# Optimization experiments

Hardware: AMD Instinct MI355X
Metric: run time of the kernel (lower is better)

## Reference

```python
import jax, jax.numpy as jnp
import numpy as np

B, T, C = 2, 2048, 1024
N_HEAD = 16
HEAD_DIM = C // N_HEAD


def setup_inputs() -> dict:
    key = jax.random.key(0)
    k1, k2, k3 = jax.random.split(key, 3)
    s = 1.0 / np.sqrt(C)
    return {
        "x": jax.random.normal(k1, (B, T, C), dtype=jnp.float32),
        "w_qkv": jax.random.normal(k2, (C, 3 * C), dtype=jnp.float32) * s,
        "b_qkv": jnp.zeros((3 * C,), dtype=jnp.float32),
        "w_out": jax.random.normal(k3, (C, C), dtype=jnp.float32) * s,
        "b_out": jnp.zeros((C,), dtype=jnp.float32),
    }


def reference(x, w_qkv, b_qkv, w_out, b_out):
    b, t, c = x.shape
    qkv = x @ w_qkv + b_qkv                                   # [B,T,3C]
    # Faithful to torch: view(B,T,H,3*hd).transpose(1,2) then split last dim
    qkv = qkv.reshape(b, t, N_HEAD, 3 * HEAD_DIM).transpose(0, 2, 1, 3)  # [B,H,T,3hd]
    q, k, v = jnp.split(qkv, 3, axis=-1)                      # each [B,H,T,hd]
    att = jnp.einsum("bhqd,bhkd->bhqk", q, k) / np.sqrt(HEAD_DIM)
    causal = jnp.tril(jnp.ones((t, t), dtype=bool))
    att = jnp.where(causal[None, None], att, -jnp.inf)
    att = jax.nn.softmax(att, axis=-1)                        # dropout p=0 (eval)
    y = jnp.einsum("bhqk,bhkd->bhqd", att, v)                 # [B,H,T,hd]
    y = y.transpose(0, 2, 1, 3).reshape(b, t, c)
    return y @ w_out + b_out
```

## Files before the change

kernel.cpp:

```cpp
#include <hip/hip_runtime.h>


#define T_SEQ 2048
#define C_DIM 1024
#define NH    16
#define HD    64
#define BT    4096

typedef short bf16x8 __attribute__((ext_vector_type(8)));
typedef float floatx4 __attribute__((ext_vector_type(4)));

static __device__ __forceinline__ unsigned short f2bf(float f) {
    union { float f; unsigned u; } v; v.f = f;
    unsigned u = v.u;
    return (unsigned short)((u + 0x7FFFu + ((u >> 16) & 1u)) >> 16);
}
static __device__ __forceinline__ float bf2f(unsigned short u) {
    union { unsigned u; float f; } v; v.u = ((unsigned)u) << 16; return v.f;
}

static __device__ __forceinline__ void gl2lds16(const void* g, void* l) {
    __builtin_amdgcn_global_load_lds(
        (const __attribute__((address_space(1))) unsigned int*)g,
        (__attribute__((address_space(3))) unsigned int*)l, 16, 0, 0);
}

static __device__ __forceinline__ void transpose_body(float (*tile)[65],
                                                      const float* __restrict__ W,
                                                      unsigned short* __restrict__ Wt,
                                                      int K, int N, int bx, int by) {
    const int k0 = by << 6;
    const int n0 = bx << 6;
    const int rr = threadIdx.x >> 4;
    const int cc = (threadIdx.x & 15) << 2;
#pragma unroll
    for (int i = 0; i < 4; i++) {
        int r = rr + (i << 4);
        *(float4*)&tile[r][cc] = *(const float4*)(W + (size_t)(k0 + r) * N + n0 + cc);
    }
    __syncthreads();
#pragma unroll
    for (int i = 0; i < 4; i++) {
        int nr = rr + (i << 4);
        ushort4 o;
        o.x = f2bf(tile[cc + 0][nr]);
        o.y = f2bf(tile[cc + 1][nr]);
        o.z = f2bf(tile[cc + 2][nr]);
        o.w = f2bf(tile[cc + 3][nr]);
        *(ushort4*)(Wt + (size_t)(n0 + nr) * K + k0 + cc) = o;
    }
}

__global__ __launch_bounds__(256) void prep(const float* __restrict__ x,
                                            unsigned short* __restrict__ xb,
                                            const float* __restrict__ w_qkv,
                                            unsigned short* __restrict__ wqkvT,
                                            const float* __restrict__ w_out,
                                            unsigned short* __restrict__ woutT) {
    __shared__ float tile[64][65];
    const int bx = blockIdx.x;
    if (bx < 1024) {
        int i = (bx * 256 + threadIdx.x) * 4;
        const int n = BT * C_DIM;
        const int stride = 1024 * 1024;
        for (; i < n; i += stride) {
            float4 f = *(const float4*)(x + i);
            ushort4 o;
            o.x = f2bf(f.x); o.y = f2bf(f.y); o.z = f2bf(f.z); o.w = f2bf(f.w);
            *(ushort4*)(xb + i) = o;
        }
    } else if (bx < 1024 + 768) {
        int b = bx - 1024;
        transpose_body(tile, w_qkv, wqkvT, 1024, 3072, b % 48, b / 48);
    } else {
        int b = bx - 1024 - 768;
        transpose_body(tile, w_out, woutT, 1024, 1024, b % 16, b / 16);
    }
}

__global__ __launch_bounds__(256) void transp_v(const unsigned short* __restrict__ vb,
                                                unsigned short* __restrict__ vt) {
    __shared__ unsigned short tile[64][68];
    const int t0 = blockIdx.x << 6;
    const int bh = blockIdx.y;
    const size_t base = (size_t)bh * T_SEQ * HD;
    const int r = threadIdx.x >> 3;
    const int c = (threadIdx.x & 7) << 3;
#pragma unroll
    for (int i = 0; i < 2; i++) {
        const unsigned short* src = vb + base + (size_t)(t0 + r + (i << 5)) * HD + c;
        ushort4 u0 = *(const ushort4*)src;
        ushort4 u1 = *(const ushort4*)(src + 4);
        *(ushort4*)&tile[r + (i << 5)][c] = u0;
        *(ushort4*)&tile[r + (i << 5)][c + 4] = u1;
    }
    __syncthreads();
#pragma unroll
    for (int i = 0; i < 2; i++) {
        int s = threadIdx.x + (i << 8);
        int d = s >> 3;
        int tc = (s & 7) << 3;
        ushort4 o0, o1;
        o0.x = tile[tc + 0][d]; o0.y = tile[tc + 1][d];
        o0.z = tile[tc + 2][d]; o0.w = tile[tc + 3][d];
        o1.x = tile[tc + 4][d]; o1.y = tile[tc + 5][d];
        o1.z = tile[tc + 6][d]; o1.w = tile[tc + 7][d];
        unsigned short* dst = vt + ((size_t)bh * HD + d) * T_SEQ + t0 + tc;
        *(ushort4*)dst = o0;
        *(ushort4*)(dst + 4) = o1;
    }
}

#define GEMM_CORE(A_, Bt_, K_)                                                      \
    __shared__ short As[128 * 64];                                                  \
    __shared__ short Bs[128 * 64];                                                  \
    const int tid  = threadIdx.x;                                                   \
    const int lane = tid & 63, wave = tid >> 6;                                     \
    const int ln   = lane & 15, quad = lane >> 4;                                   \
    const int wm   = wave & 1,  wn   = wave >> 1;                                   \
    const int row0 = blockIdx.y << 7;                                               \
    const int col0 = blockIdx.x << 7;                                               \
    floatx4 acc[4][4];                                                              \
    _Pragma("unroll")                                                               \
    for (int i = 0; i < 4; i++)                                                     \
        _Pragma("unroll")                                                           \
        for (int j = 0; j < 4; j++) acc[i][j] = (floatx4){0.f, 0.f, 0.f, 0.f};      \
    for (int k0 = 0; k0 < K_; k0 += 64) {                                           \
        _Pragma("unroll")                                                           \
        for (int i = 0; i < 4; i++) {                                               \
            int c = (i << 8) + tid;                                                 \
            int r = c >> 3;                                                         \
            int gsrc = (c & 7) ^ (r & 7);                                           \
            gl2lds16(A_  + (size_t)(row0 + r) * K_ + k0 + (gsrc << 3), &As[c << 3]); \
            gl2lds16(Bt_ + (size_t)(col0 + r) * K_ + k0 + (gsrc << 3), &Bs[c << 3]); \
        }                                                                           \
        __syncthreads();                                                            \
        _Pragma("unroll")                                                           \
        for (int half = 0; half < 2; half++) {                                      \
            bf16x8 af[4], bfr[4];                                                   \
            _Pragma("unroll")                                                       \
            for (int t4 = 0; t4 < 4; t4++) {                                        \
                int ra = (wm << 6) + (t4 << 4) + ln;                                \
                int rb = (wn << 6) + (t4 << 4) + ln;                                \
                int g  = (half << 2) + quad;                                        \
                af[t4]  = *(bf16x8*)&As[((ra << 3) + (g ^ (ra & 7))) << 3];         \
                bfr[t4] = *(bf16x8*)&Bs[((rb << 3) + (g ^ (rb & 7))) << 3];         \
            }                                                                       \
            _Pragma("unroll")                                                       \
            for (int mt = 0; mt < 4; mt++)                                          \
                _Pragma("unroll")                                                   \
                for (int nt = 0; nt < 4; nt++)                                      \
                    acc[mt][nt] = __builtin_amdgcn_mfma_f32_16x16x32_bf16(af[mt], bfr[nt], acc[mt][nt], 0, 0, 0); \
        }                                                                           \
        __syncthreads();                                                            \
    }

__global__ __launch_bounds__(256) void gemm_qkv(const unsigned short* __restrict__ A,
                                                const unsigned short* __restrict__ Bt,
                                                const float* __restrict__ bias,
                                                unsigned short* __restrict__ qb,
                                                unsigned short* __restrict__ kb,
                                                unsigned short* __restrict__ vb) {
    GEMM_CORE(A, Bt, 1024)
#pragma unroll
    for (int mt = 0; mt < 4; mt++) {
#pragma unroll
        for (int nt = 0; nt < 4; nt++) {
            int n = col0 + (wn << 6) + (nt << 4) + ln;
            int h = n / 192, r = n % 192;
            int sel = r >> 6, d = r & 63;
            float bv = bias[n];
#pragma unroll
            for (int e = 0; e < 4; e++) {
                int m = row0 + (wm << 6) + (mt << 4) + (quad << 2) + e;
                int b = m >> 11, t = m & 2047;
                float val = acc[mt][nt][e] + bv;
                size_t idx = (((size_t)(b * NH + h)) * T_SEQ + t) * HD + d;
                if (sel == 0)
                    qb[idx] = f2bf(val * 0.125f);
                else if (sel == 1)
                    kb[idx] = f2bf(val);
                else
                    vb[idx] = f2bf(val);
            }
        }
    }
}

__global__ __launch_bounds__(256) void gemm_out(const unsigned short* __restrict__ A,
                                                const unsigned short* __restrict__ Bt,
                                                const float* __restrict__ bias,
                                                float* __restrict__ out) {
    const int K = 1024, N = 1024;
    __shared__ short As[128 * 64];
    __shared__ short Bs[64 * 64];
    const int tid  = threadIdx.x;
    const int lane = tid & 63, wave = tid >> 6;
    const int ln   = lane & 15, quad = lane >> 4;
    const int wm   = wave & 1,  wn   = wave >> 1;
    const int row0 = blockIdx.y << 7;
    const int col0 = blockIdx.x << 6;
    floatx4 acc[4][2];
#pragma unroll
    for (int i = 0; i < 4; i++)
#pragma unroll
        for (int j = 0; j < 2; j++) acc[i][j] = (floatx4){0.f, 0.f, 0.f, 0.f};
    for (int k0 = 0; k0 < K; k0 += 64) {
#pragma unroll
        for (int i = 0; i < 4; i++) {
            int c = (i << 8) + tid;
            int r = c >> 3;
            int gsrc = (c & 7) ^ (r & 7);
            gl2lds16(A + (size_t)(row0 + r) * K + k0 + (gsrc << 3), &As[c << 3]);
        }
#pragma unroll
        for (int i = 0; i < 2; i++) {
            int c = (i << 8) + tid;
            int r = c >> 3;
            int gsrc = (c & 7) ^ (r & 7);
            gl2lds16(Bt + (size_t)(col0 + r) * K + k0 + (gsrc << 3), &Bs[c << 3]);
        }
        __syncthreads();
#pragma unroll
        for (int half = 0; half < 2; half++) {
            bf16x8 af[4], bfr[2];
#pragma unroll
            for (int t4 = 0; t4 < 4; t4++) {
                int ra = (wm << 6) + (t4 << 4) + ln;
                int g  = (half << 2) + quad;
                af[t4] = *(bf16x8*)&As[((ra << 3) + (g ^ (ra & 7))) << 3];
            }
#pragma unroll
            for (int t2 = 0; t2 < 2; t2++) {
                int rb = (wn << 5) + (t2 << 4) + ln;
                int g  = (half << 2) + quad;
                bfr[t2] = *(bf16x8*)&Bs[((rb << 3) + (g ^ (rb & 7))) << 3];
            }
#pragma unroll
            for (int mt = 0; mt < 4; mt++)
#pragma unroll
                for (int nt = 0; nt < 2; nt++)
                    acc[mt][nt] = __builtin_amdgcn_mfma_f32_16x16x32_bf16(af[mt], bfr[nt], acc[mt][nt], 0, 0, 0);
        }
        __syncthreads();
    }
#pragma unroll
    for (int mt = 0; mt < 4; mt++) {
#pragma unroll
        for (int nt = 0; nt < 2; nt++) {
            int n = col0 + (wn << 5) + (nt << 4) + ln;
            float bv = bias[n];
#pragma unroll
            for (int e = 0; e < 4; e++) {
                int m = row0 + (wm << 6) + (mt << 4) + (quad << 2) + e;
                out[(size_t)m * N + n] = acc[mt][nt][e] + bv;
            }
        }
    }
}

__global__ __launch_bounds__(256) void attn_p1(const unsigned short* __restrict__ qb,
                                               const unsigned short* __restrict__ kb,
                                               const unsigned short* __restrict__ vt,
                                               unsigned short* __restrict__ y,
                                               unsigned short* __restrict__ po,
                                               float* __restrict__ pm,
                                               float* __restrict__ pl) {
    __shared__ short Ks[64][68];
    __shared__ short Vs[64][68];
    __shared__ short QP[64][68];
    const int tid  = threadIdx.x;
    const int w    = tid >> 6, lane = tid & 63;
    const int ln   = lane & 15, quad = lane >> 4;
    const int bx   = blockIdx.x;
    int qt, c;
    if (bx < 32)      { qt = 31 - bx;        c = 0; }
    else if (bx < 56) { qt = 31 - (bx - 32); c = 1; }
    else if (bx < 72) { qt = 31 - (bx - 56); c = 2; }
    else              { qt = 31 - (bx - 72); c = 3; }
    const int kt_lo = c << 3;
    const int kt_hi = (kt_lo + 7 < qt) ? (kt_lo + 7) : qt;
    const int nc    = (qt >> 3) + 1;
    const bool fin  = (nc == 1);
    const int bh   = blockIdx.y;
    const size_t base = (size_t)bh * T_SEQ * HD;
    const int q0   = qt << 6;
    const int sb   = q0 + (w << 4);
    const float NEG_INF = -__builtin_inff();

    const int sr = tid >> 3;
    const int sc = (tid & 7) << 3;

    const unsigned short* qrow = qb + base + (size_t)(q0 + (w << 4) + ln) * HD;
    bf16x8 bq0 = *(const bf16x8*)(qrow + (quad << 3));
    bf16x8 bq1 = *(const bf16x8*)(qrow + 32 + (quad << 3));

    bf16x8 kreg[2], vreg[2];
    const int kk0 = kt_lo << 6;
#pragma unroll
    for (int i = 0; i < 2; i++) {
        kreg[i] = *(const bf16x8*)(kb + base + (size_t)(kk0 + sr + (i << 5)) * HD + sc);
        vreg[i] = *(const bf16x8*)(vt + base + (size_t)(sr + (i << 5)) * T_SEQ + kk0 + sc);
    }

    floatx4 o[4];
#pragma unroll
    for (int nt = 0; nt < 4; nt++) o[nt] = (floatx4){0.f, 0.f, 0.f, 0.f};
    float m_prev = NEG_INF, l_run = 0.f;

    for (int kt = kt_lo; kt <= kt_hi; kt++) {
        const int k0 = kt << 6;
        __syncthreads();
#pragma unroll
        for (int i = 0; i < 2; i++) {
            *(bf16x8*)&Ks[sr + (i << 5)][sc] = kreg[i];
            *(bf16x8*)&Vs[sr + (i << 5)][sc] = vreg[i];
        }
        __syncthreads();
        if (kt < kt_hi) {
            const int kn = k0 + 64;
#pragma unroll
            for (int i = 0; i < 2; i++) {
                kreg[i] = *(const bf16x8*)(kb + base + (size_t)(kn + sr + (i << 5)) * HD + sc);
                vreg[i] = *(const bf16x8*)(vt + base + (size_t)(sr + (i << 5)) * T_SEQ + kn + sc);
            }
        }

        const bool diag  = (kt == qt);
        const int  nlive = diag ? w : 3;

        floatx4 st[4];
#pragma unroll
        for (int ktl = 0; ktl < 4; ktl++) {
            if (ktl <= nlive) {
                bf16x8 a0 = *(bf16x8*)&Ks[(ktl << 4) + ln][quad << 3];
                bf16x8 a1 = *(bf16x8*)&Ks[(ktl << 4) + ln][32 + (quad << 3)];
                floatx4 acc = (floatx4){0.f, 0.f, 0.f, 0.f};
                acc = __builtin_amdgcn_mfma_f32_16x16x32_bf16(a0, bq0, acc, 0, 0, 0);
                acc = __builtin_amdgcn_mfma_f32_16x16x32_bf16(a1, bq1, acc, 0, 0, 0);
                st[ktl] = acc;
            }
        }
        if (diag) {
#pragma unroll
            for (int ktl = 0; ktl < 4; ktl++) {
                if (ktl <= nlive) {
#pragma unroll
                    for (int e = 0; e < 4; e++) {
                        int kg = k0 + (ktl << 4) + (quad << 2) + e;
                        if (kg > sb + ln) st[ktl][e] = NEG_INF;
                    }
                }
            }
        }

        float mx = NEG_INF;
#pragma unroll
        for (int ktl = 0; ktl < 4; ktl++)
            if (ktl <= nlive) {
#pragma unroll
                for (int e = 0; e < 4; e++) mx = fmaxf(mx, st[ktl][e]);
            }
        mx = fmaxf(mx, __shfl_xor(mx, 16));
        mx = fmaxf(mx, __shfl_xor(mx, 32));
        float m_new = fmaxf(m_prev, mx);
        float alpha = __expf(m_prev - m_new);
        float psum = 0.f;
#pragma unroll
        for (int ktl = 0; ktl < 4; ktl++)
            if (ktl <= nlive) {
#pragma unroll
                for (int e = 0; e < 4; e++) {
                    float p = __expf(st[ktl][e] - m_new);
                    st[ktl][e] = p;
                    psum += p;
                }
            }
        psum += __shfl_xor(psum, 16);
        psum += __shfl_xor(psum, 32);
        l_run = l_run * alpha + psum;
        m_prev = m_new;

#pragma unroll
        for (int ktl = 0; ktl < 4; ktl++) {
            ushort4 pw;
            if (ktl <= nlive) {
                pw.x = f2bf(st[ktl][0]); pw.y = f2bf(st[ktl][1]);
                pw.z = f2bf(st[ktl][2]); pw.w = f2bf(st[ktl][3]);
            } else {
                pw.x = 0; pw.y = 0; pw.z = 0; pw.w = 0;
            }
            *(ushort4*)&QP[(w << 4) + ln][(ktl << 4) + (quad << 2)] = pw;
        }

        float arow[4];
#pragma unroll
        for (int e = 0; e < 4; e++) arow[e] = __shfl(alpha, (quad << 2) + e);
#pragma unroll
        for (int nt = 0; nt < 4; nt++)
#pragma unroll
            for (int e = 0; e < 4; e++) o[nt][e] *= arow[e];

        bf16x8 ap0 = *(bf16x8*)&QP[(w << 4) + ln][quad << 3];
        bf16x8 ap1 = *(bf16x8*)&QP[(w << 4) + ln][32 + (quad << 3)];
#pragma unroll
        for (int nt = 0; nt < 4; nt++) {
            bf16x8 v0 = *(bf16x8*)&Vs[(nt << 4) + ln][quad << 3];
            bf16x8 v1 = *(bf16x8*)&Vs[(nt << 4) + ln][32 + (quad << 3)];
            o[nt] = __builtin_amdgcn_mfma_f32_16x16x32_bf16(ap0, v0, o[nt], 0, 0, 0);
            o[nt] = __builtin_amdgcn_mfma_f32_16x16x32_bf16(ap1, v1, o[nt], 0, 0, 0);
        }
    }

    if (fin) {
        float linv[4];
#pragma unroll
        for (int e = 0; e < 4; e++) linv[e] = 1.0f / __shfl(l_run, (quad << 2) + e);
        const int b = bh >> 4, h = bh & 15;
#pragma unroll
        for (int e = 0; e < 4; e++) {
            int t = sb + (quad << 2) + e;
            unsigned short* yrow = y + ((size_t)b * T_SEQ + t) * C_DIM + h * HD;
#pragma unroll
            for (int nt = 0; nt < 4; nt++)
                yrow[(nt << 4) + ln] = f2bf(o[nt][e] * linv[e]);
        }
    } else {
        int cb;
        if (qt < 16)      cb = (qt - 8) * 2;
        else if (qt < 24) cb = 16 + (qt - 16) * 3;
        else              cb = 40 + (qt - 24) * 4;
        const int slot = bh * 72 + cb + c;
        if (quad == 0) {
            pm[(slot << 6) + (w << 4) + ln] = m_prev;
            pl[(slot << 6) + (w << 4) + ln] = l_run;
        }
#pragma unroll
        for (int e = 0; e < 4; e++) {
            int q = (w << 4) + (quad << 2) + e;
            unsigned short* porow = po + (((size_t)slot << 6) + q) * HD;
#pragma unroll
            for (int nt = 0; nt < 4; nt++)
                porow[(nt << 4) + ln] = f2bf(o[nt][e]);
        }
    }
}

__global__ __launch_bounds__(256) void attn_p2(const unsigned short* __restrict__ po,
                                               const float* __restrict__ pm,
                                               const float* __restrict__ pl,
                                               unsigned short* __restrict__ y) {
    const int qt = 8 + blockIdx.x;
    const int bh = blockIdx.y;
    const int nc = (qt >> 3) + 1;
    int cb;
    if (qt < 16)      cb = (qt - 8) * 2;
    else if (qt < 24) cb = 16 + (qt - 16) * 3;
    else              cb = 40 + (qt - 24) * 4;
    const int slot0 = bh * 72 + cb;
    const int tid = threadIdx.x;
    const int q  = tid >> 2;
    const int d0 = (tid & 3) << 4;
    const float NEG_INF = -__builtin_inff();

    float mv[4], lv[4];
#pragma unroll
    for (int cc = 0; cc < 4; cc++) {
        if (cc < nc) {
            mv[cc] = pm[((slot0 + cc) << 6) + q];
            lv[cc] = pl[((slot0 + cc) << 6) + q];
        } else {
            mv[cc] = NEG_INF; lv[cc] = 0.f;
        }
    }
    float m = fmaxf(fmaxf(mv[0], mv[1]), fmaxf(mv[2], mv[3]));
    float a[4];
    float L = 0.f;
#pragma unroll
    for (int cc = 0; cc < 4; cc++) {
        a[cc] = __expf(mv[cc] - m);
        L += lv[cc] * a[cc];
    }
    const float inv = 1.0f / L;
#pragma unroll
    for (int cc = 0; cc < 4; cc++) a[cc] *= inv;

    float acc[16];
#pragma unroll
    for (int i = 0; i < 16; i++) acc[i] = 0.f;
#pragma unroll
    for (int cc = 0; cc < 4; cc++) {
        if (cc < nc) {
            const unsigned short* r = po + (((size_t)(slot0 + cc)) << 12) + (q << 6) + d0;
            const float ac = a[cc];
#pragma unroll
            for (int i = 0; i < 4; i++) {
                ushort4 u = *(const ushort4*)(r + (i << 2));
                acc[(i << 2) + 0] += ac * bf2f(u.x);
                acc[(i << 2) + 1] += ac * bf2f(u.y);
                acc[(i << 2) + 2] += ac * bf2f(u.z);
                acc[(i << 2) + 3] += ac * bf2f(u.w);
            }
        }
    }

    const int b = bh >> 4, h = bh & 15;
    const int t = (qt << 6) + q;
    unsigned short* yrow = y + ((size_t)b * T_SEQ + t) * C_DIM + h * HD + d0;
#pragma unroll
    for (int i = 0; i < 4; i++) {
        ushort4 ow;
        ow.x = f2bf(acc[(i << 2) + 0]);
        ow.y = f2bf(acc[(i << 2) + 1]);
        ow.z = f2bf(acc[(i << 2) + 2]);
        ow.w = f2bf(acc[(i << 2) + 3]);
        *(ushort4*)(yrow + (i << 2)) = ow;
    }
}

extern "C" void kernel_launch(void* const* d_in, const int* in_sizes, int n_in,
                              void* d_out, int out_size, void* d_ws, size_t ws_size,
                              hipStream_t stream) {
    (void)in_sizes; (void)n_in; (void)out_size; (void)ws_size;
    const float* x     = (const float*)d_in[0];
    const float* w_qkv = (const float*)d_in[1];
    const float* b_qkv = (const float*)d_in[2];
    const float* w_out = (const float*)d_in[3];
    const float* b_out = (const float*)d_in[4];
    float* out = (float*)d_out;

    char* ws = (char*)d_ws;
    unsigned short* qb    = (unsigned short*)ws;
    unsigned short* kb    = (unsigned short*)(ws + ((size_t)8  << 20));
    unsigned short* vt    = (unsigned short*)(ws + ((size_t)16 << 20));
    unsigned short* xb    = (unsigned short*)(ws + ((size_t)24 << 20));
    unsigned short* yb    = xb;
    unsigned short* woutT = (unsigned short*)(ws + ((size_t)32 << 20));
    unsigned short* vb    = (unsigned short*)(ws + ((size_t)34 << 20));
    unsigned short* wqkvT = (unsigned short*)(ws + ((size_t)42 << 20));
    unsigned short* po    = (unsigned short*)(ws + ((size_t)34 << 20));
    float*          pm    = (float*)(ws + ((size_t)52 << 20));
    float*          pl    = (float*)(ws + ((size_t)52 << 20) + (640 << 10));

    prep    <<<2048, 256, 0, stream>>>(x, xb, w_qkv, wqkvT, w_out, woutT);
    gemm_qkv<<<dim3(24, 32), 256, 0, stream>>>(xb, wqkvT, b_qkv, qb, kb, vb);
    transp_v<<<dim3(32, 32), 256, 0, stream>>>(vb, vt);
    attn_p1 <<<dim3(80, 32), 256, 0, stream>>>(qb, kb, vt, yb, po, pm, pl);
    attn_p2 <<<dim3(24, 32), 256, 0, stream>>>(po, pm, pl, yb);
    gemm_out<<<dim3(16, 32), 256, 0, stream>>>(yb, woutT, b_out, out);
}
```

Before: 206.7 us.

## Process two query tiles per attention block to reuse K/V tiles

Each attention block now handles 128 query rows (two 64-row sub-tiles) against every loaded K/V tile, which halves global K/V loads and LDS staging per query. The grid shrinks from 80x32 to 40x32 blocks, and the split-KV partial layout and combine kernel are re-indexed for 128-row slots. In exchange, register pressure goes up from the doubled accumulators and there are fewer blocks to spread across the GPU's compute units.

```diff
diff --git a/kernel.cpp b/kernel.cpp
--- a/kernel.cpp
+++ b/kernel.cpp
@@ -268,32 +268,36 @@
                                                float* __restrict__ pl) {
     __shared__ short Ks[64][68];
     __shared__ short Vs[64][68];
-    __shared__ short QP[64][68];
+    __shared__ short QP[2][64][68];
     const int tid  = threadIdx.x;
     const int w    = tid >> 6, lane = tid & 63;
     const int ln   = lane & 15, quad = lane >> 4;
     const int bx   = blockIdx.x;
-    int qt, c;
-    if (bx < 32)      { qt = 31 - bx;        c = 0; }
-    else if (bx < 56) { qt = 31 - (bx - 32); c = 1; }
-    else if (bx < 72) { qt = 31 - (bx - 56); c = 2; }
-    else              { qt = 31 - (bx - 72); c = 3; }
+    int qt2, c;
+    if (bx < 16)      { qt2 = 15 - bx;        c = 0; }
+    else if (bx < 28) { qt2 = 15 - (bx - 16); c = 1; }
+    else if (bx < 36) { qt2 = 15 - (bx - 28); c = 2; }
+    else              { qt2 = 15 - (bx - 36); c = 3; }
     const int kt_lo = c << 3;
-    const int kt_hi = (kt_lo + 7 < qt) ? (kt_lo + 7) : qt;
-    const int nc    = (qt >> 3) + 1;
+    const int qtB   = (qt2 << 1) + 1;
+    const int kt_hi = (kt_lo + 7 < qtB) ? (kt_lo + 7) : qtB;
+    const int nc    = ((qt2 << 1) + 9) >> 3;
     const bool fin  = (nc == 1);
     const int bh   = blockIdx.y;
     const size_t base = (size_t)bh * T_SEQ * HD;
-    const int q0   = qt << 6;
-    const int sb   = q0 + (w << 4);
+    const int q0   = qt2 << 7;
     const float NEG_INF = -__builtin_inff();
 
     const int sr = tid >> 3;
     const int sc = (tid & 7) << 3;
 
-    const unsigned short* qrow = qb + base + (size_t)(q0 + (w << 4) + ln) * HD;
-    bf16x8 bq0 = *(const bf16x8*)(qrow + (quad << 3));
-    bf16x8 bq1 = *(const bf16x8*)(qrow + 32 + (quad << 3));
+    bf16x8 bq[2][2];
+#pragma unroll
+    for (int s = 0; s < 2; s++) {
+        const unsigned short* qrow = qb + base + (size_t)(q0 + (s << 6) + (w << 4) + ln) * HD;
+        bq[s][0] = *(const bf16x8*)(qrow + (quad << 3));
+        bq[s][1] = *(const bf16x8*)(qrow + 32 + (quad << 3));
+    }
 
     bf16x8 kreg[2], vreg[2];
     const int kk0 = kt_lo << 6;
@@ -303,10 +307,13 @@
         vreg[i] = *(const bf16x8*)(vt + base + (size_t)(sr + (i << 5)) * T_SEQ + kk0 + sc);
     }
 
-    floatx4 o[4];
-#pragma unroll
-    for (int nt = 0; nt < 4; nt++) o[nt] = (floatx4){0.f, 0.f, 0.f, 0.f};
-    float m_prev = NEG_INF, l_run = 0.f;
+    floatx4 o[2][4];
+#pragma unroll
+    for (int s = 0; s < 2; s++)
+#pragma unroll
+        for (int nt = 0; nt < 4; nt++) o[s][nt] = (floatx4){0.f, 0.f, 0.f, 0.f};
+    float m_prev[2] = {NEG_INF, NEG_INF};
+    float l_run[2]  = {0.f, 0.f};
 
     for (int kt = kt_lo; kt <= kt_hi; kt++) {
         const int k0 = kt << 6;
@@ -326,122 +333,134 @@
             }
         }
 
-        const bool diag  = (kt == qt);
-        const int  nlive = diag ? w : 3;
-
-        floatx4 st[4];
-#pragma unroll
-        for (int ktl = 0; ktl < 4; ktl++) {
-            if (ktl <= nlive) {
-                bf16x8 a0 = *(bf16x8*)&Ks[(ktl << 4) + ln][quad << 3];
-                bf16x8 a1 = *(bf16x8*)&Ks[(ktl << 4) + ln][32 + (quad << 3)];
-                floatx4 acc = (floatx4){0.f, 0.f, 0.f, 0.f};
-                acc = __builtin_amdgcn_mfma_f32_16x16x32_bf16(a0, bq0, acc, 0, 0, 0);
-                acc = __builtin_amdgcn_mfma_f32_16x16x32_bf16(a1, bq1, acc, 0, 0, 0);
-                st[ktl] = acc;
-            }
-        }
-        if (diag) {
+#pragma unroll
+        for (int s = 0; s < 2; s++) {
+            const int qts = (qt2 << 1) + s;
+            if (kt > qts) continue;
+            const bool diag  = (kt == qts);
+            const int  nlive = diag ? w : 3;
+            const int  sb    = q0 + (s << 6) + (w << 4);
+
+            floatx4 st[4];
 #pragma unroll
             for (int ktl = 0; ktl < 4; ktl++) {
                 if (ktl <= nlive) {
-#pragma unroll
-                    for (int e = 0; e < 4; e++) {
-                        int kg = k0 + (ktl << 4) + (quad << 2) + e;
-                        if (kg > sb + ln) st[ktl][e] = NEG_INF;
+                    bf16x8 a0 = *(bf16x8*)&Ks[(ktl << 4) + ln][quad << 3];
+                    bf16x8 a1 = *(bf16x8*)&Ks[(ktl << 4) + ln][32 + (quad << 3)];
+                    floatx4 acc = (floatx4){0.f, 0.f, 0.f, 0.f};
+                    acc = __builtin_amdgcn_mfma_f32_16x16x32_bf16(a0, bq[s][0], acc, 0, 0, 0);
+                    acc = __builtin_amdgcn_mfma_f32_16x16x32_bf16(a1, bq[s][1], acc, 0, 0, 0);
+                    st[ktl] = acc;
+                }
+            }
+            if (diag) {
+#pragma unroll
+                for (int ktl = 0; ktl < 4; ktl++) {
+                    if (ktl <= nlive) {
+#pragma unroll
+                        for (int e = 0; e < 4; e++) {
+                            int kg = k0 + (ktl << 4) + (quad << 2) + e;
+                            if (kg > sb + ln) st[ktl][e] = NEG_INF;
+                        }
                     }
                 }
             }
-        }
-
-        float mx = NEG_INF;
-#pragma unroll
-        for (int ktl = 0; ktl < 4; ktl++)
-            if (ktl <= nlive) {
-#pragma unroll
-                for (int e = 0; e < 4; e++) mx = fmaxf(mx, st[ktl][e]);
-            }
-        mx = fmaxf(mx, __shfl_xor(mx, 16));
-        mx = fmaxf(mx, __shfl_xor(mx, 32));
-        float m_new = fmaxf(m_prev, mx);
-        float alpha = __expf(m_prev - m_new);
-        float psum = 0.f;
-#pragma unroll
-        for (int ktl = 0; ktl < 4; ktl++)
-            if (ktl <= nlive) {
-#pragma unroll
-                for (int e = 0; e < 4; e++) {
-                    float p = __expf(st[ktl][e] - m_new);
-                    st[ktl][e] = p;
-                    psum += p;
+
+            float mx = NEG_INF;
+#pragma unroll
+            for (int ktl = 0; ktl < 4; ktl++)
+                if (ktl <= nlive) {
+#pragma unroll
+                    for (int e = 0; e < 4; e++) mx = fmaxf(mx, st[ktl][e]);
                 }
-            }
-        psum += __shfl_xor(psum, 16);
-        psum += __shfl_xor(psum, 32);
-        l_run = l_run * alpha + psum;
-        m_prev = m_new;
-
-#pragma unroll
-        for (int ktl = 0; ktl < 4; ktl++) {
-            ushort4 pw;
-            if (ktl <= nlive) {
-                pw.x = f2bf(st[ktl][0]); pw.y = f2bf(st[ktl][1]);
-                pw.z = f2bf(st[ktl][2]); pw.w = f2bf(st[ktl][3]);
-            } else {
-                pw.x = 0; pw.y = 0; pw.z = 0; pw.w = 0;
-            }
-            *(ushort4*)&QP[(w << 4) + ln][(ktl << 4) + (quad << 2)] = pw;
-        }
-
-        float arow[4];
-#pragma unroll
-        for (int e = 0; e < 4; e++) arow[e] = __shfl(alpha, (quad << 2) + e);
-#pragma unroll
-        for (int nt = 0; nt < 4; nt++)
-#pragma unroll
-            for (int e = 0; e < 4; e++) o[nt][e] *= arow[e];
-
-        bf16x8 ap0 = *(bf16x8*)&QP[(w << 4) + ln][quad << 3];
-        bf16x8 ap1 = *(bf16x8*)&QP[(w << 4) + ln][32 + (quad << 3)];
-#pragma unroll
-        for (int nt = 0; nt < 4; nt++) {
-            bf16x8 v0 = *(bf16x8*)&Vs[(nt << 4) + ln][quad << 3];
-            bf16x8 v1 = *(bf16x8*)&Vs[(nt << 4) + ln][32 + (quad << 3)];
-            o[nt] = __builtin_amdgcn_mfma_f32_16x16x32_bf16(ap0, v0, o[nt], 0, 0, 0);
-            o[nt] = __builtin_amdgcn_mfma_f32_16x16x32_bf16(ap1, v1, o[nt], 0, 0, 0);
+            mx = fmaxf(mx, __shfl_xor(mx, 16));
+            mx = fmaxf(mx, __shfl_xor(mx, 32));
+            float m_new = fmaxf(m_prev[s], mx);
+            float alpha = __expf(m_prev[s] - m_new);
+            float psum = 0.f;
+#pragma unroll
+            for (int ktl = 0; ktl < 4; ktl++)
+                if (ktl <= nlive) {
+#pragma unroll
+                    for (int e = 0; e < 4; e++) {
+                        float p = __expf(st[ktl][e] - m_new);
+                        st[ktl][e] = p;
+                        psum += p;
+                    }
+                }
+            psum += __shfl_xor(psum, 16);
+            psum += __shfl_xor(psum, 32);
+            l_run[s] = l_run[s] * alpha + psum;
+            m_prev[s] = m_new;
+
+#pragma unroll
+            for (int ktl = 0; ktl < 4; ktl++) {
+                ushort4 pw;
+                if (ktl <= nlive) {
+                    pw.x = f2bf(st[ktl][0]); pw.y = f2bf(st[ktl][1]);
+                    pw.z = f2bf(st[ktl][2]); pw.w = f2bf(st[ktl][3]);
+                } else {
+                    pw.x = 0; pw.y = 0; pw.z = 0; pw.w = 0;
+                }
+                *(ushort4*)&QP[s][(w << 4) + ln][(ktl << 4) + (quad << 2)] = pw;
+            }
+
+            float arow[4];
+#pragma unroll
+            for (int e = 0; e < 4; e++) arow[e] = __shfl(alpha, (quad << 2) + e);
+#pragma unroll
+            for (int nt = 0; nt < 4; nt++)
+#pragma unroll
+                for (int e = 0; e < 4; e++) o[s][nt][e] *= arow[e];
+
+            bf16x8 ap0 = *(bf16x8*)&QP[s][(w << 4) + ln][quad << 3];
+            bf16x8 ap1 = *(bf16x8*)&QP[s][(w << 4) + ln][32 + (quad << 3)];
+#pragma unroll
+            for (int nt = 0; nt < 4; nt++) {
+                bf16x8 v0 = *(bf16x8*)&Vs[(nt << 4) + ln][quad << 3];
+                bf16x8 v1 = *(bf16x8*)&Vs[(nt << 4) + ln][32 + (quad << 3)];
+                o[s][nt] = __builtin_amdgcn_mfma_f32_16x16x32_bf16(ap0, v0, o[s][nt], 0, 0, 0);
+                o[s][nt] = __builtin_amdgcn_mfma_f32_16x16x32_bf16(ap1, v1, o[s][nt], 0, 0, 0);
+            }
         }
     }
 
     if (fin) {
-        float linv[4];
-#pragma unroll
-        for (int e = 0; e < 4; e++) linv[e] = 1.0f / __shfl(l_run, (quad << 2) + e);
         const int b = bh >> 4, h = bh & 15;
 #pragma unroll
-        for (int e = 0; e < 4; e++) {
-            int t = sb + (quad << 2) + e;
-            unsigned short* yrow = y + ((size_t)b * T_SEQ + t) * C_DIM + h * HD;
-#pragma unroll
-            for (int nt = 0; nt < 4; nt++)
-                yrow[(nt << 4) + ln] = f2bf(o[nt][e] * linv[e]);
+        for (int s = 0; s < 2; s++) {
+            float linv[4];
+#pragma unroll
+            for (int e = 0; e < 4; e++) linv[e] = 1.0f / __shfl(l_run[s], (quad << 2) + e);
+#pragma unroll
+            for (int e = 0; e < 4; e++) {
+                int t = q0 + (s << 6) + (w << 4) + (quad << 2) + e;
+                unsigned short* yrow = y + ((size_t)b * T_SEQ + t) * C_DIM + h * HD;
+#pragma unroll
+                for (int nt = 0; nt < 4; nt++)
+                    yrow[(nt << 4) + ln] = f2bf(o[s][nt][e] * linv[e]);
+            }
         }
     } else {
         int cb;
-        if (qt < 16)      cb = (qt - 8) * 2;
-        else if (qt < 24) cb = 16 + (qt - 16) * 3;
-        else              cb = 40 + (qt - 24) * 4;
-        const int slot = bh * 72 + cb + c;
-        if (quad == 0) {
-            pm[(slot << 6) + (w << 4) + ln] = m_prev;
-            pl[(slot << 6) + (w << 4) + ln] = l_run;
-        }
-#pragma unroll
-        for (int e = 0; e < 4; e++) {
-            int q = (w << 4) + (quad << 2) + e;
-            unsigned short* porow = po + (((size_t)slot << 6) + q) * HD;
-#pragma unroll
-            for (int nt = 0; nt < 4; nt++)
-                porow[(nt << 4) + ln] = f2bf(o[nt][e]);
+        if (qt2 < 8)       cb = (qt2 - 4) * 2;
+        else if (qt2 < 12) cb = 8 + (qt2 - 8) * 3;
+        else               cb = 20 + (qt2 - 12) * 4;
+        const int slot = bh * 36 + cb + c;
+#pragma unroll
+        for (int s = 0; s < 2; s++) {
+            if (quad == 0) {
+                pm[(slot << 7) + (s << 6) + (w << 4) + ln] = m_prev[s];
+                pl[(slot << 7) + (s << 6) + (w << 4) + ln] = l_run[s];
+            }
+#pragma unroll
+            for (int e = 0; e < 4; e++) {
+                int r = (s << 6) + (w << 4) + (quad << 2) + e;
+                unsigned short* porow = po + ((size_t)slot << 13) + (r << 6);
+#pragma unroll
+                for (int nt = 0; nt < 4; nt++)
+                    porow[(nt << 4) + ln] = f2bf(o[s][nt][e]);
+            }
         }
     }
 }
@@ -450,71 +469,74 @@
                                                const float* __restrict__ pm,
                                                const float* __restrict__ pl,
                                                unsigned short* __restrict__ y) {
-    const int qt = 8 + blockIdx.x;
-    const int bh = blockIdx.y;
-    const int nc = (qt >> 3) + 1;
+    const int qt2 = 4 + blockIdx.x;
+    const int bh  = blockIdx.y;
+    const int nc  = ((qt2 << 1) + 9) >> 3;
     int cb;
-    if (qt < 16)      cb = (qt - 8) * 2;
-    else if (qt < 24) cb = 16 + (qt - 16) * 3;
-    else              cb = 40 + (qt - 24) * 4;
-    const int slot0 = bh * 72 + cb;
+    if (qt2 < 8)       cb = (qt2 - 4) * 2;
+    else if (qt2 < 12) cb = 8 + (qt2 - 8) * 3;
+    else               cb = 20 + (qt2 - 12) * 4;
+    const int slot0 = bh * 36 + cb;
     const int tid = threadIdx.x;
-    const int q  = tid >> 2;
-    const int d0 = (tid & 3) << 4;
+    const int d0  = (tid & 3) << 4;
+    const int b = bh >> 4, h = bh & 15;
     const float NEG_INF = -__builtin_inff();
 
-    float mv[4], lv[4];
-#pragma unroll
-    for (int cc = 0; cc < 4; cc++) {
-        if (cc < nc) {
-            mv[cc] = pm[((slot0 + cc) << 6) + q];
-            lv[cc] = pl[((slot0 + cc) << 6) + q];
-        } else {
-            mv[cc] = NEG_INF; lv[cc] = 0.f;
-        }
-    }
-    float m = fmaxf(fmaxf(mv[0], mv[1]), fmaxf(mv[2], mv[3]));
-    float a[4];
-    float L = 0.f;
-#pragma unroll
-    for (int cc = 0; cc < 4; cc++) {
-        a[cc] = __expf(mv[cc] - m);
-        L += lv[cc] * a[cc];
-    }
-    const float inv = 1.0f / L;
-#pragma unroll
-    for (int cc = 0; cc < 4; cc++) a[cc] *= inv;
-
-    float acc[16];
-#pragma unroll
-    for (int i = 0; i < 16; i++) acc[i] = 0.f;
-#pragma unroll
-    for (int cc = 0; cc < 4; cc++) {
-        if (cc < nc) {
-            const unsigned short* r = po + (((size_t)(slot0 + cc)) << 12) + (q << 6) + d0;
-            const float ac = a[cc];
-#pragma unroll
-            for (int i = 0; i < 4; i++) {
-                ushort4 u = *(const ushort4*)(r + (i << 2));
-                acc[(i << 2) + 0] += ac * bf2f(u.x);
-                acc[(i << 2) + 1] += ac * bf2f(u.y);
-                acc[(i << 2) + 2] += ac * bf2f(u.z);
-                acc[(i << 2) + 3] += ac * bf2f(u.w);
-            }
-        }
-    }
-
-    const int b = bh >> 4, h = bh & 15;
-    const int t = (qt << 6) + q;
-    unsigned short* yrow = y + ((size_t)b * T_SEQ + t) * C_DIM + h * HD + d0;
-#pragma unroll
-    for (int i = 0; i < 4; i++) {
-        ushort4 ow;
-        ow.x = f2bf(acc[(i << 2) + 0]);
-        ow.y = f2bf(acc[(i << 2) + 1]);
-        ow.z = f2bf(acc[(i << 2) + 2]);
-        ow.w = f2bf(acc[(i << 2) + 3]);
-        *(ushort4*)(yrow + (i << 2)) = ow;
+#pragma unroll
+    for (int qh = 0; qh < 2; qh++) {
+        const int q = (tid >> 2) + (qh << 6);
+        float mv[4], lv[4];
+#pragma unroll
+        for (int cc = 0; cc < 4; cc++) {
+            if (cc < nc) {
+                mv[cc] = pm[((slot0 + cc) << 7) + q];
+                lv[cc] = pl[((slot0 + cc) << 7) + q];
+            } else {
+                mv[cc] = NEG_INF; lv[cc] = 0.f;
+            }
+        }
+        float m = fmaxf(fmaxf(mv[0], mv[1]), fmaxf(mv[2], mv[3]));
+        float a[4];
+        float L = 0.f;
+#pragma unroll
+        for (int cc = 0; cc < 4; cc++) {
+            a[cc] = __expf(mv[cc] - m);
+            L += lv[cc] * a[cc];
+        }
+        const float inv = 1.0f / L;
+#pragma unroll
+        for (int cc = 0; cc < 4; cc++) a[cc] *= inv;
+
+        float acc[16];
+#pragma unroll
+        for (int i = 0; i < 16; i++) acc[i] = 0.f;
+#pragma unroll
+        for (int cc = 0; cc < 4; cc++) {
+            if (cc < nc) {
+                const unsigned short* r = po + ((size_t)(slot0 + cc) << 13) + (q << 6) + d0;
+                const float ac = a[cc];
+#pragma unroll
+                for (int i = 0; i < 4; i++) {
+                    ushort4 u = *(const ushort4*)(r + (i << 2));
+                    acc[(i << 2) + 0] += ac * bf2f(u.x);
+                    acc[(i << 2) + 1] += ac * bf2f(u.y);
+                    acc[(i << 2) + 2] += ac * bf2f(u.z);
+                    acc[(i << 2) + 3] += ac * bf2f(u.w);
+                }
+            }
+        }
+
+        const int t = (qt2 << 7) + q;
+        unsigned short* yrow = y + ((size_t)b * T_SEQ + t) * C_DIM + h * HD + d0;
+#pragma unroll
+        for (int i = 0; i < 4; i++) {
+            ushort4 ow;
+            ow.x = f2bf(acc[(i << 2) + 0]);
+            ow.y = f2bf(acc[(i << 2) + 1]);
+            ow.z = f2bf(acc[(i << 2) + 2]);
+            ow.w = f2bf(acc[(i << 2) + 3]);
+            *(ushort4*)(yrow + (i << 2)) = ow;
+        }
     }
 }
 
@@ -545,7 +567,7 @@
     prep    <<<2048, 256, 0, stream>>>(x, xb, w_qkv, wqkvT, w_out, woutT);
     gemm_qkv<<<dim3(24, 32), 256, 0, stream>>>(xb, wqkvT, b_qkv, qb, kb, vb);
     transp_v<<<dim3(32, 32), 256, 0, stream>>>(vb, vt);
-    attn_p1 <<<dim3(80, 32), 256, 0, stream>>>(qb, kb, vt, yb, po, pm, pl);
-    attn_p2 <<<dim3(24, 32), 256, 0, stream>>>(po, pm, pl, yb);
+    attn_p1 <<<dim3(40, 32), 256, 0, stream>>>(qb, kb, vt, yb, po, pm, pl);
+    attn_p2 <<<dim3(12, 32), 256, 0, stream>>>(po, pm, pl, yb);
     gemm_out<<<dim3(16, 32), 256, 0, stream>>>(yb, woutT, b_out, out);
 }
```

Result: slower. 223.9 us (+8.3%).
